# Kernel optimization log

Measured on AMD Instinct MI355X. Metric: run time of the kernel, lower is better.

## Reference

```python
import jax, jax.numpy as jnp
import numpy as np

C = 256          # embed_dim
NH = 8           # n_heads
NL = 4           # n_levels
NP = 4           # n_points
HD = C // NH     # head dim = 32
SS = np.array([[128, 128], [64, 64], [32, 32], [16, 16]], dtype=np.int64)  # (H_l, W_l)
LSI = np.concatenate([[0], np.cumsum(SS[:, 0] * SS[:, 1])[:-1]]).astype(np.int64)
LIN = int((SS[:, 0] * SS[:, 1]).sum())  # 21760
B = 2
LQ = LIN


def setup_inputs() -> dict:
    key = jax.random.key(0)
    ks = jax.random.split(key, 8)
    s = 0.02
    return {
        "query": jax.random.normal(ks[0], (B, LQ, C), jnp.float32),
        "reference_points": jax.random.uniform(ks[1], (B, LQ, NL, 2), dtype=jnp.float32),
        "input_flatten": jax.random.normal(ks[2], (B, LIN, C), jnp.float32),
        "W_value": jax.random.normal(ks[3], (C, C), jnp.float32) * s,
        "b_value": jnp.zeros((C,), jnp.float32),
        "W_off": jax.random.normal(ks[4], (C, NH * NL * NP * 2), jnp.float32) * s,
        "b_off": jnp.zeros((NH * NL * NP * 2,), jnp.float32),
        "W_attn": jax.random.normal(ks[5], (C, NH * NL * NP), jnp.float32) * s,
        "b_attn": jnp.zeros((NH * NL * NP,), jnp.float32),
        "W_out": jax.random.normal(ks[6], (C, C), jnp.float32) * s,
        "b_out": jnp.zeros((C,), jnp.float32),
        "input_spatial_shapes": jnp.asarray(SS),
        "input_level_start_index": jnp.asarray(LSI),
    }


def _msda(query, reference_points, input_flatten,
          W_value, b_value, W_off, b_off, W_attn, b_attn, W_out, b_out):
    N, Lq, _ = query.shape
    Lin = input_flatten.shape[1]
    # projections
    value = (input_flatten @ W_value + b_value).reshape(N, Lin, NH, HD)
    off = (query @ W_off + b_off).reshape(N, Lq, NH, NL, NP, 2)
    aw = jax.nn.softmax((query @ W_attn + b_attn).reshape(N, Lq, NH, NL * NP), axis=-1)
    aw = aw.reshape(N, Lq, NH, NL, NP)
    # normalizer is (W_l, H_l) per level
    norm = jnp.asarray(SS[:, ::-1].copy(), jnp.float32)  # (NL, 2)
    loc = reference_points[:, :, None, :, None, :] + off / norm[None, None, None, :, None, :]
    out = jnp.zeros((N, Lq, NH, HD), query.dtype)
    for l in range(NL):
        Hl, Wl = int(SS[l, 0]), int(SS[l, 1])
        st = int(LSI[l])
        v = value[:, st:st + Hl * Wl].transpose(0, 2, 1, 3)  # (N, NH, HW, HD)
        # grid_sample align_corners=False semantics: pixel = loc*size - 0.5
        x = loc[:, :, :, l, :, 0] * Wl - 0.5  # (N, Lq, NH, NP)
        y = loc[:, :, :, l, :, 1] * Hl - 0.5
        x0 = jnp.floor(x)
        y0 = jnp.floor(y)
        lw = x - x0
        lh = y - y0
        x0i = x0.astype(jnp.int32)
        y0i = y0.astype(jnp.int32)

        def corner(ix, iy, w):
            valid = (ix >= 0) & (ix < Wl) & (iy >= 0) & (iy < Hl)
            idx = jnp.clip(iy * Wl + ix, 0, Hl * Wl - 1)
            idx_t = idx.transpose(0, 2, 1, 3).reshape(N, NH, Lq * NP)
            g = jnp.take_along_axis(v, idx_t[:, :, :, None], axis=2)
            g = g.reshape(N, NH, Lq, NP, HD)
            wt = (w * valid).transpose(0, 2, 1, 3)  # (N, NH, Lq, NP)
            return g * wt[..., None]

        samp = (corner(x0i, y0i, (1 - lw) * (1 - lh))
                + corner(x0i + 1, y0i, lw * (1 - lh))
                + corner(x0i, y0i + 1, (1 - lw) * lh)
                + corner(x0i + 1, y0i + 1, lw * lh))
        out = out + jnp.einsum('nhqpd,nqhp->nqhd', samp, aw[:, :, :, l])
    return out.reshape(N, Lq, C) @ W_out + b_out


def reference(query, reference_points, input_flatten,
              W_value, b_value, W_off, b_off, W_attn, b_attn, W_out, b_out,
              input_spatial_shapes, input_level_start_index):
    return _msda(query, reference_points, input_flatten,
                 W_value, b_value, W_off, b_off, W_attn, b_attn, W_out, b_out)
```

## Files before the change

### kernel.cpp

```cpp
#include <hip/hip_runtime.h>

typedef unsigned short u16;
typedef unsigned int u32;
typedef short bf16x8 __attribute__((ext_vector_type(8)));
typedef float f32x4 __attribute__((ext_vector_type(4)));

#define LQ_ 21760
#define LIN_ 21760
#define CDIM 256

__device__ __forceinline__ u16 f2bf(float f) {
  u32 u;
  __builtin_memcpy(&u, &f, 4);
  u32 r = (u + 0x7fffu + ((u >> 16) & 1u)) >> 16;
  return (u16)r;
}
__device__ __forceinline__ u32 pack_bf16_rne(float a, float b) {
  return (u32)f2bf(a) | ((u32)f2bf(b) << 16);
}
__device__ __forceinline__ float bflo(u32 u) {
  u32 v = u << 16;
  float f;
  __builtin_memcpy(&f, &v, 4);
  return f;
}
__device__ __forceinline__ float bfhi(u32 u) {
  u32 v = u & 0xffff0000u;
  float f;
  __builtin_memcpy(&f, &v, 4);
  return f;
}

__device__ __forceinline__ void conv_one(const float* W0, const float* W1, u16* Wf,
                                         int N, int split, int blk, int t) {
  const int tid = blk * 256 + t;
  if (tid >= N * 32) return;
  const int n = tid >> 5, kcg = tid & 31;
  float w[8];
#pragma unroll
  for (int j = 0; j < 8; ++j) {
    const int k = kcg * 8 + j;
    w[j] = (n < split) ? W0[(size_t)k * split + n]
                       : W1[(size_t)k * (N - split) + (n - split)];
  }
  uint4 pk;
  pk.x = pack_bf16_rne(w[0], w[1]);
  pk.y = pack_bf16_rne(w[2], w[3]);
  pk.z = pack_bf16_rne(w[4], w[5]);
  pk.w = pack_bf16_rne(w[6], w[7]);
  const int ks = kcg >> 2, kcr = kcg & 3, c = n >> 4;
  const int chunk = ks * (N / 4) + c * 4 + kcr;
  *(uint4*)(Wf + (size_t)chunk * 128 + (n & 15) * 8) = pk;
}

__global__ __launch_bounds__(256) void conv_all(
    const float* __restrict__ Wv, const float* __restrict__ Wof,
    const float* __restrict__ Wa, const float* __restrict__ Wo,
    const float* __restrict__ bof, const float* __restrict__ ba,
    u16* __restrict__ WfV, u16* __restrict__ WfC, u16* __restrict__ WfO,
    float* __restrict__ bcat) {
  const int b = blockIdx.x, t = threadIdx.x;
  if (b < 32) {
    conv_one(Wv, Wv, WfV, 256, 256, b, t);
  } else if (b < 80) {
    conv_one(Wof, Wa, WfC, 384, 256, b - 32, t);
  } else if (b < 112) {
    conv_one(Wo, Wo, WfO, 256, 256, b - 80, t);
  } else {
    const int i = (b - 112) * 256 + t;
    if (i < 384) bcat[i] = (i < 256) ? bof[i] : ba[i - 256];
  }
}


__global__ __launch_bounds__(256) void gemm_value(
    const float* __restrict__ A, const u16* __restrict__ Wf,
    const float* __restrict__ bias, u16* __restrict__ out) {
  __shared__ u16 sA[128 * 32];
  __shared__ u16 sB[128 * 32];
  const int rb = blockIdx.x >> 1, cb = blockIdx.x & 1;
  const int r0 = rb * 128;
  const int t = threadIdx.x, l = t & 63, wv = t >> 6;
  const int wr = wv >> 1, wc = wv & 1;
  const int fq = l >> 4, fr = l & 15;
  f32x4 acc[4][4];
#pragma unroll
  for (int r = 0; r < 4; ++r)
#pragma unroll
    for (int c = 0; c < 4; ++c) acc[r][c] = f32x4{0.f, 0.f, 0.f, 0.f};
  const int ar = t >> 1, kh = t & 1;
  u16* sA0 = sA + ((ar >> 4) * 4 + kh * 2) * 128 + (ar & 15) * 8;
  for (int ks = 0; ks < 8; ++ks) {
    __syncthreads();
    const float* ap = A + (size_t)(r0 + ar) * CDIM + ks * 32 + kh * 16;
    const float4 f0 = *(const float4*)ap;
    const float4 f1 = *(const float4*)(ap + 4);
    const float4 f2 = *(const float4*)(ap + 8);
    const float4 f3 = *(const float4*)(ap + 12);
    uint4 p0, p1;
    p0.x = pack_bf16_rne(f0.x, f0.y);
    p0.y = pack_bf16_rne(f0.z, f0.w);
    p0.z = pack_bf16_rne(f1.x, f1.y);
    p0.w = pack_bf16_rne(f1.z, f1.w);
    p1.x = pack_bf16_rne(f2.x, f2.y);
    p1.y = pack_bf16_rne(f2.z, f2.w);
    p1.z = pack_bf16_rne(f3.x, f3.y);
    p1.w = pack_bf16_rne(f3.z, f3.w);
    *(uint4*)sA0 = p0;
    *(uint4*)(sA0 + 128) = p1;
    const u16* wsrc = Wf + ((size_t)ks * 64 + cb * 32) * 128 + t * 16;
    *(uint4*)(sB + t * 16) = *(const uint4*)wsrc;
    *(uint4*)(sB + t * 16 + 8) = *(const uint4*)(wsrc + 8);
    __syncthreads();
    bf16x8 af[4];
#pragma unroll
    for (int r = 0; r < 4; ++r)
      af[r] = *(const bf16x8*)(sA + ((wr * 4 + r) * 4 + fq) * 128 + fr * 8);
#pragma unroll
    for (int c = 0; c < 4; ++c) {
      const bf16x8 bf = *(const bf16x8*)(sB + ((wc * 4 + c) * 4 + fq) * 128 + fr * 8);
#pragma unroll
      for (int r = 0; r < 4; ++r)
        acc[r][c] = __builtin_amdgcn_mfma_f32_16x16x32_bf16(af[r], bf, acc[r][c], 0, 0, 0);
    }
  }
  const int rq = fq * 4;
#pragma unroll
  for (int c = 0; c < 4; ++c) {
    const int col = cb * 128 + wc * 64 + c * 16 + fr;
    const float bz = bias[col];
#pragma unroll
    for (int r = 0; r < 4; ++r) {
      const int row0 = r0 + wr * 64 + r * 16 + rq;
#pragma unroll
      for (int g = 0; g < 4; ++g)
        out[(size_t)(row0 + g) * 256 + col] = f2bf(acc[r][c][g] + bz);
    }
  }
}

__global__ __launch_bounds__(256) void gemm_qc(
    const float* __restrict__ A, const u16* __restrict__ Wf,
    const float* __restrict__ bias, float* __restrict__ outO,
    float* __restrict__ outA) {
  __shared__ u16 sA[128 * 32];
  __shared__ u16 sB[128 * 32];
  const int rb = blockIdx.x / 3, cb = blockIdx.x % 3;
  const int r0 = rb * 128;
  const int t = threadIdx.x, l = t & 63, wv = t >> 6;
  const int wr = wv >> 1, wc = wv & 1;
  const int fq = l >> 4, fr = l & 15;
  f32x4 acc[4][4];
#pragma unroll
  for (int r = 0; r < 4; ++r)
#pragma unroll
    for (int c = 0; c < 4; ++c) acc[r][c] = f32x4{0.f, 0.f, 0.f, 0.f};
  const int ar = t >> 1, kh = t & 1;
  u16* sA0 = sA + ((ar >> 4) * 4 + kh * 2) * 128 + (ar & 15) * 8;
  for (int ks = 0; ks < 8; ++ks) {
    __syncthreads();
    const float* ap = A + (size_t)(r0 + ar) * CDIM + ks * 32 + kh * 16;
    const float4 f0 = *(const float4*)ap;
    const float4 f1 = *(const float4*)(ap + 4);
    const float4 f2 = *(const float4*)(ap + 8);
    const float4 f3 = *(const float4*)(ap + 12);
    uint4 p0, p1;
    p0.x = pack_bf16_rne(f0.x, f0.y);
    p0.y = pack_bf16_rne(f0.z, f0.w);
    p0.z = pack_bf16_rne(f1.x, f1.y);
    p0.w = pack_bf16_rne(f1.z, f1.w);
    p1.x = pack_bf16_rne(f2.x, f2.y);
    p1.y = pack_bf16_rne(f2.z, f2.w);
    p1.z = pack_bf16_rne(f3.x, f3.y);
    p1.w = pack_bf16_rne(f3.z, f3.w);
    *(uint4*)sA0 = p0;
    *(uint4*)(sA0 + 128) = p1;
    const u16* wsrc = Wf + ((size_t)ks * 96 + cb * 32) * 128 + t * 16;
    *(uint4*)(sB + t * 16) = *(const uint4*)wsrc;
    *(uint4*)(sB + t * 16 + 8) = *(const uint4*)(wsrc + 8);
    __syncthreads();
    bf16x8 af[4];
#pragma unroll
    for (int r = 0; r < 4; ++r)
      af[r] = *(const bf16x8*)(sA + ((wr * 4 + r) * 4 + fq) * 128 + fr * 8);
#pragma unroll
    for (int c = 0; c < 4; ++c) {
      const bf16x8 bf = *(const bf16x8*)(sB + ((wc * 4 + c) * 4 + fq) * 128 + fr * 8);
#pragma unroll
      for (int r = 0; r < 4; ++r)
        acc[r][c] = __builtin_amdgcn_mfma_f32_16x16x32_bf16(af[r], bf, acc[r][c], 0, 0, 0);
    }
  }
  const int rq = fq * 4;
#pragma unroll
  for (int c = 0; c < 4; ++c) {
    const int col = cb * 128 + wc * 64 + c * 16 + fr;
    const float bz = bias[col];
#pragma unroll
    for (int r = 0; r < 4; ++r) {
      const int row0 = r0 + wr * 64 + r * 16 + rq;
#pragma unroll
      for (int g = 0; g < 4; ++g) {
        const float v = acc[r][c][g] + bz;
        if (col < 256)
          outO[(size_t)(row0 + g) * 256 + col] = v;
        else
          outA[(size_t)(row0 + g) * 128 + (col - 256)] = v;
      }
    }
  }
}

__global__ __launch_bounds__(256) void gemm_out(
    const u16* __restrict__ A, const u16* __restrict__ Wf,
    const float* __restrict__ bias, float* __restrict__ out) {
  __shared__ u16 sA[128 * 32];
  __shared__ u16 sB[128 * 32];
  const int rb = blockIdx.x >> 1, cb = blockIdx.x & 1;
  const int r0 = rb * 128;
  const int t = threadIdx.x, l = t & 63, wv = t >> 6;
  const int wr = wv >> 1, wc = wv & 1;
  const int fq = l >> 4, fr = l & 15;
  f32x4 acc[4][4];
#pragma unroll
  for (int r = 0; r < 4; ++r)
#pragma unroll
    for (int c = 0; c < 4; ++c) acc[r][c] = f32x4{0.f, 0.f, 0.f, 0.f};
  const int ar = t >> 1, kh = t & 1;
  u16* sA0 = sA + ((ar >> 4) * 4 + kh * 2) * 128 + (ar & 15) * 8;
  for (int ks = 0; ks < 8; ++ks) {
    __syncthreads();
    const u16* ap = A + (size_t)(r0 + ar) * CDIM + ks * 32 + kh * 16;
    const uint4 p0 = *(const uint4*)ap;
    const uint4 p1 = *(const uint4*)(ap + 8);
    *(uint4*)sA0 = p0;
    *(uint4*)(sA0 + 128) = p1;
    const u16* wsrc = Wf + ((size_t)ks * 64 + cb * 32) * 128 + t * 16;
    *(uint4*)(sB + t * 16) = *(const uint4*)wsrc;
    *(uint4*)(sB + t * 16 + 8) = *(const uint4*)(wsrc + 8);
    __syncthreads();
    bf16x8 af[4];
#pragma unroll
    for (int r = 0; r < 4; ++r)
      af[r] = *(const bf16x8*)(sA + ((wr * 4 + r) * 4 + fq) * 128 + fr * 8);
#pragma unroll
    for (int c = 0; c < 4; ++c) {
      const bf16x8 bf = *(const bf16x8*)(sB + ((wc * 4 + c) * 4 + fq) * 128 + fr * 8);
#pragma unroll
      for (int r = 0; r < 4; ++r)
        acc[r][c] = __builtin_amdgcn_mfma_f32_16x16x32_bf16(af[r], bf, acc[r][c], 0, 0, 0);
    }
  }
  const int rq = fq * 4;
#pragma unroll
  for (int c = 0; c < 4; ++c) {
    const int col = cb * 128 + wc * 64 + c * 16 + fr;
    const float bz = bias[col];
#pragma unroll
    for (int r = 0; r < 4; ++r) {
      const int row0 = r0 + wr * 64 + r * 16 + rq;
#pragma unroll
      for (int g = 0; g < 4; ++g)
        out[(size_t)(row0 + g) * 256 + col] = acc[r][c][g] + bz;
    }
  }
}

__global__ __launch_bounds__(256) void msda_sample3(
    const u16* __restrict__ value, const float* __restrict__ off,
    const float* __restrict__ attnl, const float* __restrict__ refp,
    u16* __restrict__ out) {
  __shared__ float s_aw[64 * 17];
  __shared__ uint4 s_idx[16 * 64];
  __shared__ float4 s_w[16 * 64];
  const int t = threadIdx.x;
  const int bq0 = blockIdx.x * 8;

  if (t < 64) {
    const float* lg = attnl + (size_t)(bq0 + (t >> 3)) * 128 + (t & 7) * 16;
    float e[16];
    float m = -1e30f;
#pragma unroll
    for (int i = 0; i < 16; ++i) {
      e[i] = lg[i];
      m = fmaxf(m, e[i]);
    }
    float s = 0.f;
#pragma unroll
    for (int i = 0; i < 16; ++i) {
      e[i] = __expf(e[i] - m);
      s += e[i];
    }
    const float inv = 1.f / s;
#pragma unroll
    for (int i = 0; i < 16; ++i) s_aw[t * 17 + i] = e[i] * inv;
  }
  __syncthreads();

#pragma unroll
  for (int rr = 0; rr < 4; ++rr) {
    const int id = t + rr * 256;
    const int qh = id & 63, lp = id >> 6;
    const int q = qh >> 3, h = qh & 7, lv = lp >> 2, p = lp & 3;
    const int bq = bq0 + q;
    const int Wl = 128 >> lv;
    const int st = (lv == 0) ? 0 : (lv == 1) ? 16384 : (lv == 2) ? 20480 : 21504;
    const float ox = off[(size_t)bq * 256 + ((h * 4 + lv) * 4 + p) * 2];
    const float oy = off[(size_t)bq * 256 + ((h * 4 + lv) * 4 + p) * 2 + 1];
    const float rx = refp[(size_t)bq * 8 + lv * 2];
    const float ry = refp[(size_t)bq * 8 + lv * 2 + 1];
    const float aw = s_aw[qh * 17 + lp];
    const float x = rx * (float)Wl + ox - 0.5f;
    const float y = ry * (float)Wl + oy - 0.5f;
    const float xf = floorf(x), yf = floorf(y);
    const int x0 = (int)xf, y0 = (int)yf;
    const float lw = x - xf, lh = y - yf;
    const float hw = 1.f - lw, hh = 1.f - lh;
    const int ixs[4] = {x0, x0 + 1, x0, x0 + 1};
    const int iys[4] = {y0, y0, y0 + 1, y0 + 1};
    const float wts[4] = {hw * hh, lw * hh, hw * lh, lw * lh};
    u32 rows[4];
    float ws4[4];
#pragma unroll
    for (int c = 0; c < 4; ++c) {
      const int ix = ixs[c], iy = iys[c];
      const bool valid = (ix >= 0) & (ix < Wl) & (iy >= 0) & (iy < Wl);
      int idx = iy * Wl + ix;
      idx = max(0, min(idx, Wl * Wl - 1));
      rows[c] = (u32)(st + idx);
      ws4[c] = valid ? (wts[c] * aw) : 0.f;
    }
    uint4 iv;
    iv.x = rows[0];
    iv.y = rows[1];
    iv.z = rows[2];
    iv.w = rows[3];
    s_idx[lp * 64 + qh] = iv;
    s_w[lp * 64 + qh] = make_float4(ws4[0], ws4[1], ws4[2], ws4[3]);
  }
  __syncthreads();

  const int q = t >> 5, h = (t >> 2) & 7, dg = t & 3;
  const int qh = q * 8 + h;
  const int bq = bq0 + q;
  const u16* vp = value + (size_t)((bq >= LQ_) ? LIN_ : 0) * CDIM + h * 32 + dg * 8;
  float a0 = 0.f, a1 = 0.f, a2 = 0.f, a3 = 0.f;
  float a4 = 0.f, a5 = 0.f, a6 = 0.f, a7 = 0.f;
#pragma unroll 4
  for (int lp = 0; lp < 16; ++lp) {
    const uint4 iv = s_idx[lp * 64 + qh];
    const float4 wv = s_w[lp * 64 + qh];
    const u32 rows[4] = {iv.x, iv.y, iv.z, iv.w};
    const float ww[4] = {wv.x, wv.y, wv.z, wv.w};
#pragma unroll
    for (int c = 0; c < 4; ++c) {
      const uint4 d = *(const uint4*)(vp + (size_t)rows[c] * CDIM);
      const float w = ww[c];
      a0 += w * bflo(d.x);
      a1 += w * bfhi(d.x);
      a2 += w * bflo(d.y);
      a3 += w * bfhi(d.y);
      a4 += w * bflo(d.z);
      a5 += w * bfhi(d.z);
      a6 += w * bflo(d.w);
      a7 += w * bfhi(d.w);
    }
  }
  uint4 o;
  o.x = pack_bf16_rne(a0, a1);
  o.y = pack_bf16_rne(a2, a3);
  o.z = pack_bf16_rne(a4, a5);
  o.w = pack_bf16_rne(a6, a7);
  *(uint4*)(out + (size_t)bq * CDIM + h * 32 + dg * 8) = o;
}

extern "C" void kernel_launch(void* const* d_in, const int* in_sizes, int n_in,
                              void* d_out, int out_size, void* d_ws, size_t ws_size,
                              hipStream_t stream) {
  const float* query = (const float*)d_in[0];
  const float* refp = (const float*)d_in[1];
  const float* inflat = (const float*)d_in[2];
  const float* Wv = (const float*)d_in[3];
  const float* bv = (const float*)d_in[4];
  const float* Wof = (const float*)d_in[5];
  const float* bof = (const float*)d_in[6];
  const float* Wa = (const float*)d_in[7];
  const float* ba = (const float*)d_in[8];
  const float* Wo = (const float*)d_in[9];
  const float* bo = (const float*)d_in[10];
  float* out = (float*)d_out;

  const int M = 2 * LQ_;

  u16* ws_value = (u16*)d_ws;
  u16* ws_samp = ws_value + (size_t)M * 256;
  float* ws_off = (float*)(ws_samp + (size_t)M * 256);
  float* ws_attn = ws_off + (size_t)M * 256;
  u16* WfV = (u16*)(ws_attn + (size_t)M * 128);
  u16* WfC = WfV + 256 * 256;
  u16* WfO = WfC + 384 * 256;
  float* bcat = (float*)(WfO + 256 * 256);

  conv_all<<<dim3(114), dim3(256), 0, stream>>>(Wv, Wof, Wa, Wo, bof, ba, WfV, WfC, WfO,
                                                bcat);
  gemm_value<<<dim3(680), dim3(256), 0, stream>>>(inflat, WfV, bv, ws_value);
  gemm_qc<<<dim3(1020), dim3(256), 0, stream>>>(query, WfC, bcat, ws_off, ws_attn);
  msda_sample3<<<dim3(M / 8), dim3(256), 0, stream>>>(ws_value, ws_off, ws_attn, refp,
                                                      ws_samp);
  gemm_out<<<dim3(680), dim3(256), 0, stream>>>(ws_samp, WfO, bo, out);
}
```

Measured before the change: 292.0 us.

## Pre-convert activations to tiled bf16 and use direct global-to-LDS loads in GEMMs

Adds a conversion kernel that turns query and input_flatten into bf16 stored in the MFMA-ready tile layout. All three GEMMs then stage A and B tiles with global_load_lds instead of register round-trips. The sampling kernel packs each row index and its bf16 weight into one 32-bit entry to halve shared-memory traffic. It also remaps block order across batches and writes its output directly in the tiled layout for gemm_out. Costs are an extra conversion pass over both activations, bf16 rounding of the sampling weights, and a 16-bit row index that only fits because each batch has at most 21760 rows.

Measured after the change: 319.3 us. 1.09x slower.

```diff
diff --git a/kernel.cpp b/kernel.cpp
--- a/kernel.cpp
+++ b/kernel.cpp
@@ -8,6 +8,7 @@
 #define LQ_ 21760
 #define LIN_ 21760
 #define CDIM 256
+#define MROWS (2 * LQ_)
 
 __device__ __forceinline__ u16 f2bf(float f) {
   u32 u;
@@ -29,6 +30,10 @@
   float f;
   __builtin_memcpy(&f, &v, 4);
   return f;
+}
+__device__ __forceinline__ void ldst16(const u16* g, u16* l) {
+  __builtin_amdgcn_global_load_lds((const __attribute__((address_space(1))) void*)g,
+                                   (__attribute__((address_space(3))) void*)l, 16, 0, 0);
 }
 
 __device__ __forceinline__ void conv_one(const float* W0, const float* W1, u16* Wf,
@@ -72,14 +77,46 @@
   }
 }
 
+__global__ __launch_bounds__(256) void conv_act(const float* __restrict__ Aq,
+                                                const float* __restrict__ Ai,
+                                                u16* __restrict__ Qf,
+                                                u16* __restrict__ If) {
+  const int i = blockIdx.x * 256 + threadIdx.x;
+  const int n4 = MROWS * 32;
+  const float* src;
+  u16* dst;
+  int j;
+  if (i < n4) {
+    src = Aq;
+    dst = Qf;
+    j = i;
+  } else {
+    src = Ai;
+    dst = If;
+    j = i - n4;
+  }
+  const int tile = j >> 9;
+  const int c2 = (j >> 4) & 31;
+  const int sr = j & 15;
+  const int row = (tile >> 3) * 128 + (c2 >> 2) * 16 + sr;
+  const int kc = (tile & 7) * 32 + (c2 & 3) * 8;
+  const float4 f0 = *(const float4*)(src + (size_t)row * 256 + kc);
+  const float4 f1 = *(const float4*)(src + (size_t)row * 256 + kc + 4);
+  uint4 pk;
+  pk.x = pack_bf16_rne(f0.x, f0.y);
+  pk.y = pack_bf16_rne(f0.z, f0.w);
+  pk.z = pack_bf16_rne(f1.x, f1.y);
+  pk.w = pack_bf16_rne(f1.z, f1.w);
+  *(uint4*)(dst + (size_t)j * 8) = pk;
+}
+
 
 __global__ __launch_bounds__(256) void gemm_value(
-    const float* __restrict__ A, const u16* __restrict__ Wf,
+    const u16* __restrict__ Af, const u16* __restrict__ Wf,
     const float* __restrict__ bias, u16* __restrict__ out) {
-  __shared__ u16 sA[128 * 32];
-  __shared__ u16 sB[128 * 32];
+  __shared__ u16 sA[4096];
+  __shared__ u16 sB[4096];
   const int rb = blockIdx.x >> 1, cb = blockIdx.x & 1;
-  const int r0 = rb * 128;
   const int t = threadIdx.x, l = t & 63, wv = t >> 6;
   const int wr = wv >> 1, wc = wv & 1;
   const int fq = l >> 4, fr = l & 15;
@@ -88,29 +125,16 @@
   for (int r = 0; r < 4; ++r)
 #pragma unroll
     for (int c = 0; c < 4; ++c) acc[r][c] = f32x4{0.f, 0.f, 0.f, 0.f};
-  const int ar = t >> 1, kh = t & 1;
-  u16* sA0 = sA + ((ar >> 4) * 4 + kh * 2) * 128 + (ar & 15) * 8;
   for (int ks = 0; ks < 8; ++ks) {
     __syncthreads();
-    const float* ap = A + (size_t)(r0 + ar) * CDIM + ks * 32 + kh * 16;
-    const float4 f0 = *(const float4*)ap;
-    const float4 f1 = *(const float4*)(ap + 4);
-    const float4 f2 = *(const float4*)(ap + 8);
-    const float4 f3 = *(const float4*)(ap + 12);
-    uint4 p0, p1;
-    p0.x = pack_bf16_rne(f0.x, f0.y);
-    p0.y = pack_bf16_rne(f0.z, f0.w);
-    p0.z = pack_bf16_rne(f1.x, f1.y);
-    p0.w = pack_bf16_rne(f1.z, f1.w);
-    p1.x = pack_bf16_rne(f2.x, f2.y);
-    p1.y = pack_bf16_rne(f2.z, f2.w);
-    p1.z = pack_bf16_rne(f3.x, f3.y);
-    p1.w = pack_bf16_rne(f3.z, f3.w);
-    *(uint4*)sA0 = p0;
-    *(uint4*)(sA0 + 128) = p1;
-    const u16* wsrc = Wf + ((size_t)ks * 64 + cb * 32) * 128 + t * 16;
-    *(uint4*)(sB + t * 16) = *(const uint4*)wsrc;
-    *(uint4*)(sB + t * 16 + 8) = *(const uint4*)(wsrc + 8);
+    const u16* ga = Af + ((size_t)(rb * 8 + ks)) * 4096 + wv * 1024 + l * 8;
+    u16* la = sA + wv * 1024;
+    ldst16(ga, la);
+    ldst16(ga + 512, la + 512);
+    const u16* gb = Wf + ((size_t)(ks * 64 + cb * 32)) * 128 + wv * 1024 + l * 8;
+    u16* lb = sB + wv * 1024;
+    ldst16(gb, lb);
+    ldst16(gb + 512, lb + 512);
     __syncthreads();
     bf16x8 af[4];
 #pragma unroll
@@ -131,7 +155,7 @@
     const float bz = bias[col];
 #pragma unroll
     for (int r = 0; r < 4; ++r) {
-      const int row0 = r0 + wr * 64 + r * 16 + rq;
+      const int row0 = rb * 128 + wr * 64 + r * 16 + rq;
 #pragma unroll
       for (int g = 0; g < 4; ++g)
         out[(size_t)(row0 + g) * 256 + col] = f2bf(acc[r][c][g] + bz);
@@ -140,13 +164,12 @@
 }
 
 __global__ __launch_bounds__(256) void gemm_qc(
-    const float* __restrict__ A, const u16* __restrict__ Wf,
+    const u16* __restrict__ Af, const u16* __restrict__ Wf,
     const float* __restrict__ bias, float* __restrict__ outO,
     float* __restrict__ outA) {
-  __shared__ u16 sA[128 * 32];
-  __shared__ u16 sB[128 * 32];
+  __shared__ u16 sA[4096];
+  __shared__ u16 sB[4096];
   const int rb = blockIdx.x / 3, cb = blockIdx.x % 3;
-  const int r0 = rb * 128;
   const int t = threadIdx.x, l = t & 63, wv = t >> 6;
   const int wr = wv >> 1, wc = wv & 1;
   const int fq = l >> 4, fr = l & 15;
@@ -155,29 +178,16 @@
   for (int r = 0; r < 4; ++r)
 #pragma unroll
     for (int c = 0; c < 4; ++c) acc[r][c] = f32x4{0.f, 0.f, 0.f, 0.f};
-  const int ar = t >> 1, kh = t & 1;
-  u16* sA0 = sA + ((ar >> 4) * 4 + kh * 2) * 128 + (ar & 15) * 8;
   for (int ks = 0; ks < 8; ++ks) {
     __syncthreads();
-    const float* ap = A + (size_t)(r0 + ar) * CDIM + ks * 32 + kh * 16;
-    const float4 f0 = *(const float4*)ap;
-    const float4 f1 = *(const float4*)(ap + 4);
-    const float4 f2 = *(const float4*)(ap + 8);
-    const float4 f3 = *(const float4*)(ap + 12);
-    uint4 p0, p1;
-    p0.x = pack_bf16_rne(f0.x, f0.y);
-    p0.y = pack_bf16_rne(f0.z, f0.w);
-    p0.z = pack_bf16_rne(f1.x, f1.y);
-    p0.w = pack_bf16_rne(f1.z, f1.w);
-    p1.x = pack_bf16_rne(f2.x, f2.y);
-    p1.y = pack_bf16_rne(f2.z, f2.w);
-    p1.z = pack_bf16_rne(f3.x, f3.y);
-    p1.w = pack_bf16_rne(f3.z, f3.w);
-    *(uint4*)sA0 = p0;
-    *(uint4*)(sA0 + 128) = p1;
-    const u16* wsrc = Wf + ((size_t)ks * 96 + cb * 32) * 128 + t * 16;
-    *(uint4*)(sB + t * 16) = *(const uint4*)wsrc;
-    *(uint4*)(sB + t * 16 + 8) = *(const uint4*)(wsrc + 8);
+    const u16* ga = Af + ((size_t)(rb * 8 + ks)) * 4096 + wv * 1024 + l * 8;
+    u16* la = sA + wv * 1024;
+    ldst16(ga, la);
+    ldst16(ga + 512, la + 512);
+    const u16* gb = Wf + ((size_t)(ks * 96 + cb * 32)) * 128 + wv * 1024 + l * 8;
+    u16* lb = sB + wv * 1024;
+    ldst16(gb, lb);
+    ldst16(gb + 512, lb + 512);
     __syncthreads();
     bf16x8 af[4];
 #pragma unroll
@@ -198,7 +208,7 @@
     const float bz = bias[col];
 #pragma unroll
     for (int r = 0; r < 4; ++r) {
-      const int row0 = r0 + wr * 64 + r * 16 + rq;
+      const int row0 = rb * 128 + wr * 64 + r * 16 + rq;
 #pragma unroll
       for (int g = 0; g < 4; ++g) {
         const float v = acc[r][c][g] + bz;
@@ -212,12 +222,11 @@
 }
 
 __global__ __launch_bounds__(256) void gemm_out(
-    const u16* __restrict__ A, const u16* __restrict__ Wf,
+    const u16* __restrict__ Af, const u16* __restrict__ Wf,
     const float* __restrict__ bias, float* __restrict__ out) {
-  __shared__ u16 sA[128 * 32];
-  __shared__ u16 sB[128 * 32];
+  __shared__ u16 sA[4096];
+  __shared__ u16 sB[4096];
   const int rb = blockIdx.x >> 1, cb = blockIdx.x & 1;
-  const int r0 = rb * 128;
   const int t = threadIdx.x, l = t & 63, wv = t >> 6;
   const int wr = wv >> 1, wc = wv & 1;
   const int fq = l >> 4, fr = l & 15;
@@ -226,18 +235,16 @@
   for (int r = 0; r < 4; ++r)
 #pragma unroll
     for (int c = 0; c < 4; ++c) acc[r][c] = f32x4{0.f, 0.f, 0.f, 0.f};
-  const int ar = t >> 1, kh = t & 1;
-  u16* sA0 = sA + ((ar >> 4) * 4 + kh * 2) * 128 + (ar & 15) * 8;
   for (int ks = 0; ks < 8; ++ks) {
     __syncthreads();
-    const u16* ap = A + (size_t)(r0 + ar) * CDIM + ks * 32 + kh * 16;
-    const uint4 p0 = *(const uint4*)ap;
-    const uint4 p1 = *(const uint4*)(ap + 8);
-    *(uint4*)sA0 = p0;
-    *(uint4*)(sA0 + 128) = p1;
-    const u16* wsrc = Wf + ((size_t)ks * 64 + cb * 32) * 128 + t * 16;
-    *(uint4*)(sB + t * 16) = *(const uint4*)wsrc;
-    *(uint4*)(sB + t * 16 + 8) = *(const uint4*)(wsrc + 8);
+    const u16* ga = Af + ((size_t)(rb * 8 + ks)) * 4096 + wv * 1024 + l * 8;
+    u16* la = sA + wv * 1024;
+    ldst16(ga, la);
+    ldst16(ga + 512, la + 512);
+    const u16* gb = Wf + ((size_t)(ks * 64 + cb * 32)) * 128 + wv * 1024 + l * 8;
+    u16* lb = sB + wv * 1024;
+    ldst16(gb, lb);
+    ldst16(gb + 512, lb + 512);
     __syncthreads();
     bf16x8 af[4];
 #pragma unroll
@@ -258,7 +265,7 @@
     const float bz = bias[col];
 #pragma unroll
     for (int r = 0; r < 4; ++r) {
-      const int row0 = r0 + wr * 64 + r * 16 + rq;
+      const int row0 = rb * 128 + wr * 64 + r * 16 + rq;
 #pragma unroll
       for (int g = 0; g < 4; ++g)
         out[(size_t)(row0 + g) * 256 + col] = acc[r][c][g] + bz;
@@ -266,15 +273,15 @@
   }
 }
 
-__global__ __launch_bounds__(256) void msda_sample3(
+__global__ __launch_bounds__(256) void msda_sample4(
     const u16* __restrict__ value, const float* __restrict__ off,
     const float* __restrict__ attnl, const float* __restrict__ refp,
-    u16* __restrict__ out) {
+    u16* __restrict__ samp) {
   __shared__ float s_aw[64 * 17];
-  __shared__ uint4 s_idx[16 * 64];
-  __shared__ float4 s_w[16 * 64];
+  __shared__ uint4 s_ent[16 * 64];
   const int t = threadIdx.x;
-  const int bq0 = blockIdx.x * 8;
+  const int bid = (blockIdx.x & 7) * 680 + (blockIdx.x >> 3);
+  const int bq0 = bid * 8;
 
   if (t < 64) {
     const float* lg = attnl + (size_t)(bq0 + (t >> 3)) * 128 + (t & 7) * 16;
@@ -319,24 +326,22 @@
     const int ixs[4] = {x0, x0 + 1, x0, x0 + 1};
     const int iys[4] = {y0, y0, y0 + 1, y0 + 1};
     const float wts[4] = {hw * hh, lw * hh, hw * lh, lw * lh};
-    u32 rows[4];
-    float ws4[4];
+    u32 ent[4];
 #pragma unroll
     for (int c = 0; c < 4; ++c) {
       const int ix = ixs[c], iy = iys[c];
       const bool valid = (ix >= 0) & (ix < Wl) & (iy >= 0) & (iy < Wl);
       int idx = iy * Wl + ix;
       idx = max(0, min(idx, Wl * Wl - 1));
-      rows[c] = (u32)(st + idx);
-      ws4[c] = valid ? (wts[c] * aw) : 0.f;
-    }
-    uint4 iv;
-    iv.x = rows[0];
-    iv.y = rows[1];
-    iv.z = rows[2];
-    iv.w = rows[3];
-    s_idx[lp * 64 + qh] = iv;
-    s_w[lp * 64 + qh] = make_float4(ws4[0], ws4[1], ws4[2], ws4[3]);
+      const float w = valid ? (wts[c] * aw) : 0.f;
+      ent[c] = (u32)(st + idx) | ((u32)f2bf(w) << 16);
+    }
+    uint4 ev;
+    ev.x = ent[0];
+    ev.y = ent[1];
+    ev.z = ent[2];
+    ev.w = ent[3];
+    s_ent[lp * 64 + qh] = ev;
   }
   __syncthreads();
 
@@ -348,14 +353,13 @@
   float a4 = 0.f, a5 = 0.f, a6 = 0.f, a7 = 0.f;
 #pragma unroll 4
   for (int lp = 0; lp < 16; ++lp) {
-    const uint4 iv = s_idx[lp * 64 + qh];
-    const float4 wv = s_w[lp * 64 + qh];
-    const u32 rows[4] = {iv.x, iv.y, iv.z, iv.w};
-    const float ww[4] = {wv.x, wv.y, wv.z, wv.w};
+    const uint4 ev = s_ent[lp * 64 + qh];
+    const u32 es[4] = {ev.x, ev.y, ev.z, ev.w};
 #pragma unroll
     for (int c = 0; c < 4; ++c) {
-      const uint4 d = *(const uint4*)(vp + (size_t)rows[c] * CDIM);
-      const float w = ww[c];
+      const u32 e = es[c];
+      const float w = bfhi(e);
+      const uint4 d = *(const uint4*)(vp + (size_t)(e & 0xffffu) * CDIM);
       a0 += w * bflo(d.x);
       a1 += w * bfhi(d.x);
       a2 += w * bflo(d.y);
@@ -371,7 +375,9 @@
   o.y = pack_bf16_rne(a2, a3);
   o.z = pack_bf16_rne(a4, a5);
   o.w = pack_bf16_rne(a6, a7);
-  *(uint4*)(out + (size_t)bq * CDIM + h * 32 + dg * 8) = o;
+  const int tile = (bq >> 7) * 8 + h;
+  const int c2 = ((bq & 127) >> 4) * 4 + dg;
+  *(uint4*)(samp + ((size_t)tile * 512 + c2 * 16 + (bq & 15)) * 8) = o;
 }
 
 extern "C" void kernel_launch(void* const* d_in, const int* in_sizes, int n_in,
@@ -390,22 +396,25 @@
   const float* bo = (const float*)d_in[10];
   float* out = (float*)d_out;
 
-  const int M = 2 * LQ_;
-
-  u16* ws_value = (u16*)d_ws;
-  u16* ws_samp = ws_value + (size_t)M * 256;
-  float* ws_off = (float*)(ws_samp + (size_t)M * 256);
-  float* ws_attn = ws_off + (size_t)M * 256;
-  u16* WfV = (u16*)(ws_attn + (size_t)M * 128);
+  const size_t M = MROWS;
+
+  u16* If = (u16*)d_ws;
+  u16* Qf = If + M * 256;
+  u16* ws_value = Qf + M * 256;
+  float* ws_off = (float*)(ws_value + M * 256);
+  float* ws_attn = ws_off + M * 256;
+  u16* WfV = (u16*)(ws_attn + M * 128);
   u16* WfC = WfV + 256 * 256;
   u16* WfO = WfC + 384 * 256;
   float* bcat = (float*)(WfO + 256 * 256);
+  u16* ws_samp = If;
 
   conv_all<<<dim3(114), dim3(256), 0, stream>>>(Wv, Wof, Wa, Wo, bof, ba, WfV, WfC, WfO,
                                                 bcat);
-  gemm_value<<<dim3(680), dim3(256), 0, stream>>>(inflat, WfV, bv, ws_value);
-  gemm_qc<<<dim3(1020), dim3(256), 0, stream>>>(query, WfC, bcat, ws_off, ws_attn);
-  msda_sample3<<<dim3(M / 8), dim3(256), 0, stream>>>(ws_value, ws_off, ws_attn, refp,
-                                                      ws_samp);
+  conv_act<<<dim3(10880), dim3(256), 0, stream>>>(query, inflat, Qf, If);
+  gemm_value<<<dim3(680), dim3(256), 0, stream>>>(If, WfV, bv, ws_value);
+  gemm_qc<<<dim3(1020), dim3(256), 0, stream>>>(Qf, WfC, bcat, ws_off, ws_attn);
+  msda_sample4<<<dim3(5440), dim3(256), 0, stream>>>(ws_value, ws_off, ws_attn, refp,
+                                                     ws_samp);
   gemm_out<<<dim3(680), dim3(256), 0, stream>>>(ws_samp, WfO, bo, out);
 }
```
